# Kernel optimization log

Measured on AMD Instinct MI355X. Metric: run time of the kernel, lower is better.

## Reference

```python
import jax, jax.numpy as jnp
import numpy as np

N_CLASSES = 5
N_SAMPLES = 512
D_EMB = 512


def setup_inputs() -> dict:
    key = jax.random.key(0)
    k1, k2, k3 = jax.random.split(key, 3)
    prediction = jax.random.normal(k1, (N_SAMPLES, D_EMB), dtype=jnp.float32)
    target = jax.random.randint(k2, (N_SAMPLES,), 0, N_CLASSES)
    # learnable_map=None -> all learnable, init = inverse_softplus(0.5 + 0.5*U[0,1))
    t = 0.5 + 0.5 * jax.random.uniform(k3, (N_CLASSES - 1,), dtype=jnp.float32)
    distances_raw = jnp.log(jnp.exp(t) - 1.0)  # inverse softplus (t < 20 always)
    return {"prediction": prediction, "distances_raw": distances_raw, "target": target}


def reference(prediction, distances_raw, target):
    n = prediction.shape[0]
    eps = 1e-8  # torch F.cosine_similarity eps
    xn = prediction / jnp.maximum(jnp.linalg.norm(prediction, axis=1, keepdims=True), eps)
    cos = xn @ xn.T  # [i, j] pairwise cosine similarity

    same = target[:, None] == target[None, :]          # label_diff <= 0
    positives = same & ~jnp.eye(n, dtype=bool)          # same label, not self
    negatives = ~same                                   # different label

    # ordinal class positions from softplus-parameterized gaps
    pos_d = jax.nn.softplus(distances_raw)
    class_pos = jnp.concatenate([jnp.zeros(1, dtype=pos_d.dtype), jnp.cumsum(pos_d)])
    cp = class_pos[target]
    margins = jnp.where(negatives, jnp.abs(cp[:, None] - cp[None, :]), 0.0)  # [i, j]

    # Original loop over anchor-positive columns k:
    #   n_pair_loss[k][i, j] = -cos[i, k] + cos[i, j] + margins[i, j]
    #   valid iff positives[i, k] and negatives[i, j]; invalid -> relu(-inf)=0
    base = cos + margins                                # [i, j]
    diff = base[:, None, :] - cos[:, :, None]           # [i, k, j]
    val = jnp.where(negatives[:, None, :], jax.nn.relu(diff), 0.0)
    s = jnp.where(positives, val.sum(axis=2), 0.0)      # [i, k]
    negcount = negatives.sum(axis=1)                    # [i]
    cnt = jnp.where(positives, negcount[:, None], 0)    # loss_mask2
    L = s / jnp.maximum(cnt, 1)                         # per (anchor i, positive k)

    # mean over nonzero entries (mean_n_pair_loss[mean_n_pair_loss != 0].mean())
    nz = (L != 0.0).sum()
    return L.sum() / jnp.maximum(nz, 1).astype(L.dtype)
```

## Files before the change

### kernel.cpp

```cpp
#include <hip/hip_runtime.h>
#include <math.h>

#define NS 512
#define DE 512
#define NCL 5
#define NBLK 256


__global__ __launch_bounds__(512) void k_all(const float* __restrict__ pred,
                                             const int* __restrict__ target,
                                             const float* __restrict__ draw,
                                             float* __restrict__ psum,
                                             int* __restrict__ pnz) {
    const int b = blockIdx.x;
    const int tid = threadIdx.x;
    const int iA = b, iB = b + 256;

    __shared__ float  rn_s[NS];
    __shared__ float  ckA[NS], ckB[NS];
    __shared__ float4 v4sA[NS / 4], v4sB[NS / 4];
    __shared__ int    pkA[NS], pkB[NS];
    __shared__ float  spart[NS * 17];
    __shared__ float  redf[512];
    __shared__ int    redi[512];
    __shared__ unsigned int pcA, pcB;

    if (tid == 0) { pcA = 0u; pcB = 0u; }

    const int w = tid >> 6, lane = tid & 63;
    const int g = lane >> 4, s = lane & 15;

    const float4* pA = (const float4*)&pred[(size_t)iA * DE];
    const float4* pB = (const float4*)&pred[(size_t)iB * DE];
    float4 fA[8], fB[8];
#pragma unroll
    for (int p = 0; p < 8; p++) { fA[p] = pA[p * 16 + s]; fB[p] = pB[p * 16 + s]; }

    const float4* p4 = (const float4*)pred;
    const float4* rj0 = p4 + (size_t)(w * 64 + g) * (DE / 4);
    float4 xc[8];
#pragma unroll
    for (int p = 0; p < 8; p++) xc[p] = rj0[p * 16 + s];

#pragma unroll
    for (int t = 0; t < 16; t++) {
        float4 xn[8];
        if (t < 15) {
            const float4* rjn = rj0 + (size_t)(t + 1) * 4 * (DE / 4);
#pragma unroll
            for (int p = 0; p < 8; p++) xn[p] = rjn[p * 16 + s];
        }
        const int j = w * 64 + t * 4 + g;
        float aA = 0.0f, aB = 0.0f, aS = 0.0f;
#pragma unroll
        for (int p = 0; p < 8; p++) {
            float4 x = xc[p];
            aA = fmaf(x.x, fA[p].x, aA); aA = fmaf(x.y, fA[p].y, aA);
            aA = fmaf(x.z, fA[p].z, aA); aA = fmaf(x.w, fA[p].w, aA);
            aB = fmaf(x.x, fB[p].x, aB); aB = fmaf(x.y, fB[p].y, aB);
            aB = fmaf(x.z, fB[p].z, aB); aB = fmaf(x.w, fB[p].w, aB);
            aS = fmaf(x.x, x.x, aS);     aS = fmaf(x.y, x.y, aS);
            aS = fmaf(x.z, x.z, aS);     aS = fmaf(x.w, x.w, aS);
        }
#pragma unroll
        for (int m = 1; m <= 8; m <<= 1) {
            aA += __shfl_xor(aA, m);
            aB += __shfl_xor(aB, m);
            aS += __shfl_xor(aS, m);
        }
        if (s == 0) {
            ckA[j] = aA;
            ckB[j] = aB;
            rn_s[j] = 1.0f / fmaxf(sqrtf(aS), 1e-8f);
        }
#pragma unroll
        for (int p = 0; p < 8; p++) xc[p] = xn[p];
    }

    float cp[NCL];
    cp[0] = 0.0f;
#pragma unroll
    for (int c = 0; c < NCL - 1; c++) cp[c + 1] = cp[c] + log1pf(expf(draw[c]));
    const int tiA = target[iA], tiB = target[iB];
    const float cpA = cp[tiA], cpB = cp[tiB];
    const int j = tid;
    const int tj = target[j];
    const float cpj = cp[tj];
    __syncthreads();

    const float rniA = rn_s[iA], rniB = rn_s[iB], rnj = rn_s[j];
    {
        float c0 = ckA[j] * rniA * rnj;
        bool n0 = (tj != tiA);
        ckA[j] = c0;
        ((float*)v4sA)[j] = n0 ? (c0 + fabsf(cpA - cpj)) : -1e30f;
        if (!n0 && j != iA) pkA[atomicAdd(&pcA, 1u)] = j;
        redi[tid] = (n0 ? 1 : 0);
    }
    {
        float c0 = ckB[j] * rniB * rnj;
        bool n0 = (tj != tiB);
        ckB[j] = c0;
        ((float*)v4sB)[j] = n0 ? (c0 + fabsf(cpB - cpj)) : -1e30f;
        if (!n0 && j != iB) pkB[atomicAdd(&pcB, 1u)] = j;
        redi[tid] += (n0 ? 1 : 0) << 16;
    }
    __syncthreads();
    for (int s2 = 256; s2 > 0; s2 >>= 1) {
        if (tid < s2) redi[tid] += redi[tid + s2];
        __syncthreads();
    }
    const int negA = redi[0] & 0xffff;
    const int negB = redi[0] >> 16;
    const unsigned int nposA = pcA, nposB = pcB;
    __syncthreads();

    const int kl = tid & 31, jc = tid >> 5;
    const float denA = (float)(negA > 1 ? negA : 1);
    const float denB = (float)(negB > 1 ? negB : 1);
    float contrib = 0.0f;
    int nzc = 0;

    {
        float4 vj[8];
#pragma unroll
        for (int t = 0; t < 8; t++) vj[t] = v4sA[jc * 8 + t];
        for (unsigned int p = kl; p < nposA; p += 32) {
            const float ckp = ckA[pkA[p]];
            float s0 = 0.0f, s1 = 0.0f;
#pragma unroll
            for (int t = 0; t < 8; t++) {
                float4 wv = vj[t];
                s0 += fmaxf(wv.x - ckp, 0.0f) + fmaxf(wv.y - ckp, 0.0f);
                s1 += fmaxf(wv.z - ckp, 0.0f) + fmaxf(wv.w - ckp, 0.0f);
            }
            spart[p * 17 + jc] = s0 + s1;
        }
        __syncthreads();
        for (unsigned int p = tid; p < nposA; p += 512) {
            float s0 = 0.0f;
#pragma unroll
            for (int q = 0; q < 16; q++) s0 += spart[p * 17 + q];
            contrib += s0 / denA;
            if (s0 != 0.0f) nzc++;
        }
        __syncthreads();
    }
    {
        float4 vj[8];
#pragma unroll
        for (int t = 0; t < 8; t++) vj[t] = v4sB[jc * 8 + t];
        for (unsigned int p = kl; p < nposB; p += 32) {
            const float ckp = ckB[pkB[p]];
            float s0 = 0.0f, s1 = 0.0f;
#pragma unroll
            for (int t = 0; t < 8; t++) {
                float4 wv = vj[t];
                s0 += fmaxf(wv.x - ckp, 0.0f) + fmaxf(wv.y - ckp, 0.0f);
                s1 += fmaxf(wv.z - ckp, 0.0f) + fmaxf(wv.w - ckp, 0.0f);
            }
            spart[p * 17 + jc] = s0 + s1;
        }
        __syncthreads();
        for (unsigned int p = tid; p < nposB; p += 512) {
            float s0 = 0.0f;
#pragma unroll
            for (int q = 0; q < 16; q++) s0 += spart[p * 17 + q];
            contrib += s0 / denB;
            if (s0 != 0.0f) nzc++;
        }
    }

    redf[tid] = contrib;
    redi[tid] = nzc;
    __syncthreads();
    for (int s2 = 256; s2 > 0; s2 >>= 1) {
        if (tid < s2) { redf[tid] += redf[tid + s2]; redi[tid] += redi[tid + s2]; }
        __syncthreads();
    }
    if (tid == 0) {
        psum[b] = redf[0];
        pnz[b]  = redi[0];
    }
}

__global__ __launch_bounds__(256) void k_final(const float* __restrict__ psum,
                                               const int* __restrict__ pnz,
                                               float* __restrict__ out) {
    const int tid = threadIdx.x;
    __shared__ float rf[256];
    __shared__ int   ri[256];
    rf[tid] = psum[tid];
    ri[tid] = pnz[tid];
    __syncthreads();
    for (int s = 128; s > 0; s >>= 1) {
        if (tid < s) { rf[tid] += rf[tid + s]; ri[tid] += ri[tid + s]; }
        __syncthreads();
    }
    if (tid == 0) {
        int n = ri[0];
        out[0] = rf[0] / (float)(n > 1 ? n : 1);
    }
}

extern "C" void kernel_launch(void* const* d_in, const int* in_sizes, int n_in,
                              void* d_out, int out_size, void* d_ws, size_t ws_size,
                              hipStream_t stream) {
    const float* pred   = (const float*)d_in[0];
    const float* draw   = (const float*)d_in[1];
    const int*   target = (const int*)d_in[2];
    float* out = (float*)d_out;

    float* psum = (float*)d_ws;
    int*   pnz  = (int*)(psum + NBLK);

    hipLaunchKernelGGL(k_all, dim3(NBLK), dim3(512), 0, stream,
                       pred, target, draw, psum, pnz);
    hipLaunchKernelGGL(k_final, dim3(1), dim3(256), 0, stream, psum, pnz, out);
}
```

Before: 76.67 us.

## Use wavefront shuffle reductions, deepen row prefetch, and request two blocks per CU

Replaces the shared-memory tree reductions for the negative count and the final partial sums with wavefront shuffle reductions plus a small per-wave shared array. This removes many __syncthreads barriers. Deepens the register prefetch of prediction rows from one stage ahead to two, so global load latency is better hidden. Adds a minimum-blocks hint to launch_bounds, which may cap registers and cause spills given the larger prefetch buffers.

Result: no change. 75.88 us (-1.0%).

```diff
diff --git a/kernel.cpp b/kernel.cpp
--- a/kernel.cpp
+++ b/kernel.cpp
@@ -7,11 +7,11 @@
 #define NBLK 256
 
 
-__global__ __launch_bounds__(512) void k_all(const float* __restrict__ pred,
-                                             const int* __restrict__ target,
-                                             const float* __restrict__ draw,
-                                             float* __restrict__ psum,
-                                             int* __restrict__ pnz) {
+__global__ __launch_bounds__(512, 2) void k_all(const float* __restrict__ pred,
+                                                const int* __restrict__ target,
+                                                const float* __restrict__ draw,
+                                                float* __restrict__ psum,
+                                                int* __restrict__ pnz) {
     const int b = blockIdx.x;
     const int tid = threadIdx.x;
     const int iA = b, iB = b + 256;
@@ -21,8 +21,8 @@
     __shared__ float4 v4sA[NS / 4], v4sB[NS / 4];
     __shared__ int    pkA[NS], pkB[NS];
     __shared__ float  spart[NS * 17];
-    __shared__ float  redf[512];
-    __shared__ int    redi[512];
+    __shared__ float  wf[8];
+    __shared__ int    wi[8];
     __shared__ unsigned int pcA, pcB;
 
     if (tid == 0) { pcA = 0u; pcB = 0u; }
@@ -38,15 +38,18 @@
 
     const float4* p4 = (const float4*)pred;
     const float4* rj0 = p4 + (size_t)(w * 64 + g) * (DE / 4);
-    float4 xc[8];
-#pragma unroll
-    for (int p = 0; p < 8; p++) xc[p] = rj0[p * 16 + s];
+    const int rstep = 4 * (DE / 4);
+    float4 x0[8], x1[8];
+#pragma unroll
+    for (int p = 0; p < 8; p++) x0[p] = rj0[p * 16 + s];
+#pragma unroll
+    for (int p = 0; p < 8; p++) x1[p] = rj0[rstep + p * 16 + s];
 
 #pragma unroll
     for (int t = 0; t < 16; t++) {
         float4 xn[8];
-        if (t < 15) {
-            const float4* rjn = rj0 + (size_t)(t + 1) * 4 * (DE / 4);
+        if (t < 14) {
+            const float4* rjn = rj0 + (size_t)(t + 2) * rstep;
 #pragma unroll
             for (int p = 0; p < 8; p++) xn[p] = rjn[p * 16 + s];
         }
@@ -54,7 +57,7 @@
         float aA = 0.0f, aB = 0.0f, aS = 0.0f;
 #pragma unroll
         for (int p = 0; p < 8; p++) {
-            float4 x = xc[p];
+            float4 x = x0[p];
             aA = fmaf(x.x, fA[p].x, aA); aA = fmaf(x.y, fA[p].y, aA);
             aA = fmaf(x.z, fA[p].z, aA); aA = fmaf(x.w, fA[p].w, aA);
             aB = fmaf(x.x, fB[p].x, aB); aB = fmaf(x.y, fB[p].y, aB);
@@ -74,7 +77,7 @@
             rn_s[j] = 1.0f / fmaxf(sqrtf(aS), 1e-8f);
         }
 #pragma unroll
-        for (int p = 0; p < 8; p++) xc[p] = xn[p];
+        for (int p = 0; p < 8; p++) { x0[p] = x1[p]; x1[p] = xn[p]; }
     }
 
     float cp[NCL];
@@ -89,13 +92,14 @@
     __syncthreads();
 
     const float rniA = rn_s[iA], rniB = rn_s[iB], rnj = rn_s[j];
+    int nc;
     {
         float c0 = ckA[j] * rniA * rnj;
         bool n0 = (tj != tiA);
         ckA[j] = c0;
         ((float*)v4sA)[j] = n0 ? (c0 + fabsf(cpA - cpj)) : -1e30f;
         if (!n0 && j != iA) pkA[atomicAdd(&pcA, 1u)] = j;
-        redi[tid] = (n0 ? 1 : 0);
+        nc = (n0 ? 1 : 0);
     }
     {
         float c0 = ckB[j] * rniB * rnj;
@@ -103,17 +107,18 @@
         ckB[j] = c0;
         ((float*)v4sB)[j] = n0 ? (c0 + fabsf(cpB - cpj)) : -1e30f;
         if (!n0 && j != iB) pkB[atomicAdd(&pcB, 1u)] = j;
-        redi[tid] += (n0 ? 1 : 0) << 16;
-    }
-    __syncthreads();
-    for (int s2 = 256; s2 > 0; s2 >>= 1) {
-        if (tid < s2) redi[tid] += redi[tid + s2];
-        __syncthreads();
-    }
-    const int negA = redi[0] & 0xffff;
-    const int negB = redi[0] >> 16;
+        nc += (n0 ? 1 : 0) << 16;
+    }
+#pragma unroll
+    for (int m = 1; m <= 32; m <<= 1) nc += __shfl_xor(nc, m);
+    if ((tid & 63) == 0) wi[tid >> 6] = nc;
+    __syncthreads();
+    int negpack = 0;
+#pragma unroll
+    for (int q = 0; q < 8; q++) negpack += wi[q];
+    const int negA = negpack & 0xffff;
+    const int negB = negpack >> 16;
     const unsigned int nposA = pcA, nposB = pcB;
-    __syncthreads();
 
     const int kl = tid & 31, jc = tid >> 5;
     const float denA = (float)(negA > 1 ? negA : 1);
@@ -171,16 +176,20 @@
         }
     }
 
-    redf[tid] = contrib;
-    redi[tid] = nzc;
-    __syncthreads();
-    for (int s2 = 256; s2 > 0; s2 >>= 1) {
-        if (tid < s2) { redf[tid] += redf[tid + s2]; redi[tid] += redi[tid + s2]; }
-        __syncthreads();
-    }
+#pragma unroll
+    for (int m = 1; m <= 32; m <<= 1) {
+        contrib += __shfl_xor(contrib, m);
+        nzc     += __shfl_xor(nzc, m);
+    }
+    __syncthreads();
+    if ((tid & 63) == 0) { wf[tid >> 6] = contrib; wi[tid >> 6] = nzc; }
+    __syncthreads();
     if (tid == 0) {
-        psum[b] = redf[0];
-        pnz[b]  = redi[0];
+        float sfin = 0.0f; int nfin = 0;
+#pragma unroll
+        for (int q = 0; q < 8; q++) { sfin += wf[q]; nfin += wi[q]; }
+        psum[b] = sfin;
+        pnz[b]  = nfin;
     }
 }
 
```
